# Optimization experiments

Measured on AMD Instinct MI355X. Metric: run time of the kernel, lower is better.

The kernel has to match this reference:

```python
import jax, jax.numpy as jnp
import numpy as np

C = 256
G = 32            # GroupNorm groups = min(32, C)
DQK = C // 8      # q/k channel dim
EPS = 1e-5


def setup_inputs() -> dict:
    key = jax.random.key(0)
    ks = jax.random.split(key, 10)
    B, H, W = 4, 64, 64
    s = 0.02
    return {
        "x": jax.random.normal(ks[0], (B, C, H, W), dtype=jnp.float32),
        "gamma": jnp.ones((C,), jnp.float32),
        "beta": jnp.zeros((C,), jnp.float32),
        "wq": jax.random.normal(ks[1], (DQK, C), jnp.float32) * s,
        "bq": jnp.zeros((DQK,), jnp.float32),
        "wk": jax.random.normal(ks[2], (DQK, C), jnp.float32) * s,
        "bk": jnp.zeros((DQK,), jnp.float32),
        "wv": jax.random.normal(ks[3], (C, C), jnp.float32) * s,
        "bv": jnp.zeros((C,), jnp.float32),
        "wp": jax.random.normal(ks[4], (C, C), jnp.float32) * s,
        "bp": jnpp if False else jnp.zeros((C,), jnp.float32),
    }


def reference(x, gamma, beta, wq, bq, wk, bk, wv, bv, wp, bp):
    B, Cc, H, W = x.shape
    N = H * W
    # GroupNorm(32, C), affine
    h = x.reshape(B, G, Cc // G, H, W)
    mu = h.mean(axis=(2, 3, 4), keepdims=True)
    var = h.var(axis=(2, 3, 4), keepdims=True)
    h = (h - mu) * jax.lax.rsqrt(var + EPS)
    h = h.reshape(B, Cc, N) * gamma[:, None] + beta[:, None]
    # 1x1 convs == per-token linear maps over channels
    q = jnp.einsum('dc,bcn->bnd', wq, h) + bq            # [B, N, DQK]
    k = jnp.einsum('dc,bcn->bdn', wk, h) + bk[:, None]   # [B, DQK, N]
    v = jnp.einsum('ec,bcn->ben', wv, h) + bv[:, None]   # [B, C, N]
    scale = DQK ** (-0.5)
    attn = jax.nn.softmax(jnp.einsum('bnd,bdm->bnm', q, k) * scale, axis=-1)
    out = jnp.einsum('bnm,bem->ben', attn, v)            # [B, C, N]
    proj = jnp.einsum('fe,ben->bfn', wp, out) + bp[:, None]
    return x + proj.reshape(B, Cc, H, W)
```

## Files before the change

### kernel.cpp

```cpp
#include <hip/hip_runtime.h>
#include <hip/hip_bf16.h>

#define NB 4
#define CD 256
#define NT 4096
#define DQ 32

typedef __attribute__((ext_vector_type(8))) __bf16 bf16x8;
typedef __attribute__((ext_vector_type(16))) float float16v;
typedef __attribute__((ext_vector_type(4))) unsigned int uint4v;
typedef __attribute__((ext_vector_type(2))) unsigned int uint2v;

#if __has_builtin(__builtin_amdgcn_exp2f)
#define EXP2(x) __builtin_amdgcn_exp2f(x)
#else
#define EXP2(x) exp2f(x)
#endif

__device__ inline unsigned short f2bf(float f) {
  unsigned u = __float_as_uint(f);
  u += 0x7fffu + ((u >> 16) & 1u);
  return (unsigned short)(u >> 16);
}

#define BARRIER() asm volatile("s_waitcnt lgkmcnt(0)\n\ts_barrier" ::: "memory")

__global__ __launch_bounds__(1024) void stats_pack(
    const float* __restrict__ x, const float* __restrict__ gamma,
    const float* __restrict__ beta, const float* __restrict__ wq,
    const float* __restrict__ wk, const float* __restrict__ wv,
    const float* __restrict__ wp, const float* __restrict__ bq,
    const float* __restrict__ bk, const float* __restrict__ bv,
    float* __restrict__ sc, float* __restrict__ sh,
    unsigned short* __restrict__ wqkv, unsigned short* __restrict__ wpb,
    float* __restrict__ bias) {
  int bx = blockIdx.x;
  int tid = threadIdx.x;
  if (bx < 128) {
    int b = bx >> 5, g = bx & 31;
    const float4* xp = (const float4*)(x + (size_t)bx * 32768);
    float s = 0.f, ss = 0.f;
#pragma unroll
    for (int i = 0; i < 8; i++) {
      float4 t4 = xp[i * 1024 + tid];
      s += t4.x + t4.y + t4.z + t4.w;
      ss += t4.x * t4.x + t4.y * t4.y + t4.z * t4.z + t4.w * t4.w;
    }
#pragma unroll
    for (int off = 32; off >= 1; off >>= 1) {
      s += __shfl_xor(s, off);
      ss += __shfl_xor(ss, off);
    }
    __shared__ float red[32];
    int wid = tid >> 6;
    if ((tid & 63) == 0) {
      red[wid] = s;
      red[16 + wid] = ss;
    }
    __syncthreads();
    if (tid < 8) {
      float S = 0.f, SS = 0.f;
#pragma unroll
      for (int i = 0; i < 16; i++) {
        S += red[i];
        SS += red[16 + i];
      }
      float mu = S * (1.f / 32768.f);
      float rstd = rsqrtf(SS * (1.f / 32768.f) - mu * mu + 1e-5f);
      int c = g * 8 + tid;
      float gm = gamma[c];
      sc[b * CD + c] = gm * rstd;
      sh[b * CD + c] = beta[c] - mu * gm * rstd;
    }
  } else {
    const float scale2 = 0.2550348909867343f;
    int i = (bx - 128) * 1024 + tid;
    if (i < 320 * 256) {
      int j = i >> 8, c = i & 255;
      float v;
      if (j < 32) v = wq[j * 256 + c] * scale2;
      else if (j < 64) v = wk[(j - 32) * 256 + c];
      else v = wv[(j - 64) * 256 + c];
      wqkv[i] = f2bf(v);
    } else if (i < 320 * 256 + 256 * 256) {
      int k = i - 320 * 256;
      wpb[k] = f2bf(wp[k]);
    } else if (i < 320 * 256 + 256 * 256 + 320) {
      int j = i - (320 * 256 + 256 * 256);
      float v;
      if (j < 32) v = bq[j] * scale2;
      else if (j < 64) v = bk[j - 32];
      else v = bv[j - 64];
      bias[j] = v;
    }
  }
}

__global__ __launch_bounds__(512) void qkv_norm(
    const float* __restrict__ x, const float* __restrict__ sc,
    const float* __restrict__ sh, const unsigned short* __restrict__ A,
    const float* __restrict__ bias, unsigned short* __restrict__ qk,
    unsigned short* __restrict__ v) {
  int nt = blockIdx.x, b = blockIdx.y;
  int tid = threadIdx.x, lane = tid & 63, w = tid >> 6;
  int l31 = lane & 31, hh = lane >> 5;
  int n0 = nt * 32;

  __shared__ unsigned short Hs[32 * 262];
  const float* xb = x + (size_t)b * CD * NT + n0;
  const float* scb = sc + b * CD;
  const float* shb = sh + b * CD;
  {
    int n_l = tid & 31, cg = tid >> 5;
    int c0 = cg * 16;
    unsigned short hv[16];
#pragma unroll
    for (int j = 0; j < 16; j++) {
      float val = xb[(size_t)(c0 + j) * NT + n_l];
      hv[j] = f2bf(val * scb[c0 + j] + shb[c0 + j]);
    }
    *(uint4v*)&Hs[n_l * 262 + c0] = *(uint4v*)hv;
    *(uint4v*)&Hs[n_l * 262 + c0 + 8] = *(uint4v*)(hv + 8);
  }
  __syncthreads();

  int n = n0 + l31;
  int itg = n >> 6, sp = (n >> 4) & 3;
  int lsn = ((n >> 3) & 1) * 32;
  int el = n & 7;
  const unsigned short* Brow = &Hs[l31 * 262 + 8 * hh];
  for (int t = w; t < 10; t += 8) {
    int m_base = t * 32;
    const unsigned short* Arow = A + (size_t)(m_base + l31) * 256 + 8 * hh;
    float16v acc;
#pragma unroll
    for (int r = 0; r < 16; r++) acc[r] = 0.f;
#pragma unroll
    for (int s = 0; s < 16; s++) {
      bf16x8 af = *(const bf16x8*)(Arow + 16 * s);
      bf16x8 bf = *(const bf16x8*)(Brow + 16 * s);
      acc = __builtin_amdgcn_mfma_f32_32x32x16_bf16(af, bf, acc, 0, 0, 0);
    }
#pragma unroll
    for (int r = 0; r < 16; r++) {
      int j = m_base + (r & 3) + 8 * (r >> 2) + 4 * hh;
      float val = acc[r] + bias[j];
      if (j < 64) {
        qk[((size_t)b * NT + n) * 64 + j] = f2bf(val);
      } else {
        int e = j - 64;
        int et = e >> 5;
        v[((((size_t)b * 64 + itg) * 8 + et) * 4 + sp) * 512 +
          (lsn + (e & 31)) * 8 + el] = f2bf(val);
      }
    }
  }
}

#define K_STAGE2(TNEXT, KSW)                                                  \
  if (tid >= 256) {                                                           \
    *(uint4v*)&Ks[(KSW) * 2304 + skr * 36 + skc] = kregA;                     \
    *(uint4v*)&Ks[((KSW) + 1) * 2304 + skr * 36 + skc] = kregB;               \
    int ta_ = (TNEXT) > 31 ? 31 : (TNEXT);                                    \
    int tb_ = (TNEXT) + 1 > 31 ? 31 : (TNEXT) + 1;                            \
    kregA =                                                                   \
        *(const uint4v*)&qkb[(size_t)(mbase + ta_ * 64 + skr) * 64 + 32 + skc]; \
    kregB =                                                                   \
        *(const uint4v*)&qkb[(size_t)(mbase + tb_ * 64 + skr) * 64 + 32 + skc]; \
  }

#define QK_ONE(KSB, PBB)                                                      \
  if (w < 4) {                                                                \
    float16v st;                                                              \
    _Pragma("unroll") for (int r = 0; r < 16; r++) st[r] = 0.f;               \
    __builtin_amdgcn_s_setprio(1);                                            \
    _Pragma("unroll") for (int s = 0; s < 2; s++) {                           \
      bf16x8 af = *(const bf16x8*)&Ks[(KSB) * 2304 + (32 * ks2 + l31) * 36 +  \
                                      16 * s + 8 * hh];                       \
      st = __builtin_amdgcn_mfma_f32_32x32x16_bf16(af, qfr[s], st, 0, 0, 0);  \
    }                                                                         \
    __builtin_amdgcn_s_setprio(0);                                            \
    _Pragma("unroll") for (int rq = 0; rq < 4; rq++) {                        \
      float e0 = EXP2(st[4 * rq + 0]);                                        \
      float e1 = EXP2(st[4 * rq + 1]);                                        \
      float e2 = EXP2(st[4 * rq + 2]);                                        \
      float e3 = EXP2(st[4 * rq + 3]);                                        \
      lsum += (e0 + e1) + (e2 + e3);                                          \
      uint2v pw;                                                              \
      pw[0] = __builtin_amdgcn_perm(__float_as_uint(e1), __float_as_uint(e0), \
                                    0x07060302u);                             \
      pw[1] = __builtin_amdgcn_perm(__float_as_uint(e3), __float_as_uint(e2), \
                                    0x07060302u);                             \
      *(uint2v*)&Pbuf[(PBB) * 4352 + (qs * 32 + l31) * 68 + 8 * rq + 4 * hh + \
                      32 * ks2] = pw;                                         \
    }                                                                         \
  }

#define PV_ONE(PBB, VS)                                                       \
  {                                                                           \
    __builtin_amdgcn_s_setprio(1);                                            \
    _Pragma("unroll") for (int sp = 0; sp < 4; sp++) {                        \
      bf16x8 a0 =                                                             \
          *(const bf16x8*)&Pbuf[(PBB) * 4352 + l31 * 68 + 16 * sp + 8 * hh];  \
      bf16x8 a1 = *(const bf16x8*)&Pbuf[(PBB) * 4352 + (32 + l31) * 68 +      \
                                        16 * sp + 8 * hh];                    \
      acc[0] =                                                                \
          __builtin_amdgcn_mfma_f32_32x32x16_bf16(a0, VS[sp], acc[0], 0, 0, 0); \
      acc[1] =                                                                \
          __builtin_amdgcn_mfma_f32_32x32x16_bf16(a1, VS[sp], acc[1], 0, 0, 0); \
    }                                                                         \
    __builtin_amdgcn_s_setprio(0);                                            \
  }

#define V_LOAD2(T)                                                            \
  {                                                                           \
    const unsigned short* vp0_ = vbase + (size_t)(T)*16384;                   \
    const unsigned short* vp1_ = vbase + (size_t)((T) + 1) * 16384;           \
    _Pragma("unroll") for (int u = 0; u < 4; u++) {                           \
      vS0[u] = *(const bf16x8*)(vp0_ + u * 512);                              \
      vS1[u] = *(const bf16x8*)(vp1_ + u * 512);                              \
    }                                                                         \
  }

__global__ __launch_bounds__(512, 4) void attn_fused(
    const unsigned short* __restrict__ qk, const unsigned short* __restrict__ Vp,
    unsigned short* __restrict__ Pa, unsigned short* __restrict__ Pb,
    float* __restrict__ lp4) {
  int L = blockIdx.x;
  int xv = L & 7;
  int b = xv >> 1;
  int kh = xv & 1;
  int n0 = (L >> 3) * 64;
  int tid = threadIdx.x, lane = tid & 63, w = tid >> 6;
  int l31 = lane & 31, hh = lane >> 5;
  int qs = w & 1, ks2 = (w >> 1) & 1;

  __shared__ unsigned short Ks[4 * 2304];
  __shared__ unsigned short Pbuf[4 * 4352];

  const unsigned short* qkb = qk + (size_t)b * NT * 64;
  const unsigned short* vit = Vp + ((size_t)b * 64 + kh * 32) * 16384;
  const unsigned short* vbase = vit + (size_t)w * 4 * 512 + lane * 8;

  bf16x8 qfr[2];
  if (w < 4) {
    int n_g = n0 + 32 * qs + l31;
    qfr[0] = *(const bf16x8*)&qkb[(size_t)n_g * 64 + 8 * hh];
    qfr[1] = *(const bf16x8*)&qkb[(size_t)n_g * 64 + 8 * hh + 16];
  }

  int tK = tid - 256;
  int skr = tK >> 2, skc = (tK & 3) * 8;
  int mbase = kh * 2048;
  uint4v kregA, kregB;

  float16v acc[2];
#pragma unroll
  for (int q2 = 0; q2 < 2; q2++)
#pragma unroll
    for (int r = 0; r < 16; r++) acc[q2][r] = 0.f;
  float lsum = 0.f;

  bf16x8 vS0[4], vS1[4];
  if (tid >= 256) {
    kregA = *(const uint4v*)&qkb[(size_t)(mbase + skr) * 64 + 32 + skc];
    kregB = *(const uint4v*)&qkb[(size_t)(mbase + 64 + skr) * 64 + 32 + skc];
    *(uint4v*)&Ks[skr * 36 + skc] = kregA;
    *(uint4v*)&Ks[2304 + skr * 36 + skc] = kregB;
    kregA = *(const uint4v*)&qkb[(size_t)(mbase + 128 + skr) * 64 + 32 + skc];
    kregB = *(const uint4v*)&qkb[(size_t)(mbase + 192 + skr) * 64 + 32 + skc];
  }
  BARRIER();

  K_STAGE2(4, 2);
  QK_ONE(0, 0);
  QK_ONE(1, 1);
  V_LOAD2(0);
  BARRIER();

  for (int p = 1; p < 15; p += 2) {
    K_STAGE2(2 * p + 4, 0);
    QK_ONE(2, 2);
    QK_ONE(3, 3);
    PV_ONE(0, vS0);
    PV_ONE(1, vS1);
    V_LOAD2(2 * p);
    BARRIER();
    K_STAGE2(2 * p + 6, 2);
    QK_ONE(0, 0);
    QK_ONE(1, 1);
    PV_ONE(2, vS0);
    PV_ONE(3, vS1);
    V_LOAD2(2 * p + 2);
    BARRIER();
  }
  K_STAGE2(34, 0);
  QK_ONE(2, 2);
  QK_ONE(3, 3);
  PV_ONE(0, vS0);
  PV_ONE(1, vS1);
  V_LOAD2(30);
  BARRIER();
  PV_ONE(2, vS0);
  PV_ONE(3, vS1);

  if (w < 4) {
    lsum += __shfl_xor(lsum, 32);
    if (hh == 0) {
      lp4[(size_t)((kh * 2 + ks2) * NB + b) * NT + n0 + 32 * qs + l31] = lsum;
    }
  }

  unsigned short* Pout = (kh ? Pb : Pa) + (size_t)b * NT * CD;
#pragma unroll
  for (int r = 0; r < 16; r++) {
    int nl = (r & 3) + 8 * (r >> 2) + 4 * hh;
    Pout[(size_t)(n0 + nl) * CD + 32 * w + l31] = f2bf(acc[0][r]);
    Pout[(size_t)(n0 + 32 + nl) * CD + 32 * w + l31] = f2bf(acc[1][r]);
  }
}

__global__ __launch_bounds__(256) void proj_gemm(
    const unsigned short* __restrict__ Wp, const unsigned short* __restrict__ Pa,
    const unsigned short* __restrict__ Pb, const float* __restrict__ lp4,
    const float* __restrict__ bp, const float* __restrict__ x,
    float* __restrict__ out) {
  int nt = blockIdx.x, mh = blockIdx.y, b = blockIdx.z;
  int tid = threadIdx.x, lane = tid & 63;
  int w = tid >> 6;
  int l31 = lane & 31, hh = lane >> 5;
  int n0 = nt * 32;

  __shared__ unsigned short Bs[32 * 262];
  {
    int row = tid >> 3, c8 = (tid & 7) * 8;
    float lA = 0.f;
#pragma unroll
    for (int s4 = 0; s4 < 4; s4++)
      lA += lp4[(size_t)(s4 * NB + b) * NT + n0 + row];
    float inv = 1.f / lA;
#pragma unroll
    for (int u = 0; u < 4; u++) {
      int col = c8 + u * 64;
      size_t goff = ((size_t)b * NT + n0 + row) * CD + col;
      uint4v ua = *(const uint4v*)(Pa + goff);
      uint4v ub = *(const uint4v*)(Pb + goff);
      uint4v rr;
#pragma unroll
      for (int j = 0; j < 4; j++) {
        float lo = __uint_as_float(ua[j] << 16) + __uint_as_float(ub[j] << 16);
        float hi = __uint_as_float(ua[j] & 0xffff0000u) +
                   __uint_as_float(ub[j] & 0xffff0000u);
        lo *= inv;
        hi *= inv;
        rr[j] = __builtin_amdgcn_perm(__float_as_uint(hi), __float_as_uint(lo),
                                      0x07060302u);
      }
      *(uint4v*)&Bs[row * 262 + col] = rr;
    }
  }
  __syncthreads();

  int m_base = mh * 128 + w * 32;
  const unsigned short* Arow = Wp + (size_t)(m_base + l31) * 256 + 8 * hh;
  const unsigned short* b0p = &Bs[l31 * 262 + 8 * hh];
  float16v acc;
#pragma unroll
  for (int r = 0; r < 16; r++) acc[r] = 0.f;
#pragma unroll
  for (int s = 0; s < 16; s++) {
    bf16x8 af = *(const bf16x8*)(Arow + 16 * s);
    bf16x8 bf0 = *(const bf16x8*)(b0p + 16 * s);
    acc = __builtin_amdgcn_mfma_f32_32x32x16_bf16(af, bf0, acc, 0, 0, 0);
  }
  int n = n0 + l31;
#pragma unroll
  for (int r = 0; r < 16; r++) {
    int f = m_base + (r & 3) + 8 * (r >> 2) + 4 * hh;
    size_t idx = ((size_t)b * CD + f) * NT + n;
    out[idx] = x[idx] + acc[r] + bp[f];
  }
}

extern "C" void kernel_launch(void* const* d_in, const int* in_sizes, int n_in,
                              void* d_out, int out_size, void* d_ws,
                              size_t ws_size, hipStream_t stream) {
  (void)in_sizes; (void)n_in; (void)out_size; (void)ws_size;
  const float* x = (const float*)d_in[0];
  const float* gamma = (const float*)d_in[1];
  const float* beta = (const float*)d_in[2];
  const float* wq = (const float*)d_in[3];
  const float* bq = (const float*)d_in[4];
  const float* wk = (const float*)d_in[5];
  const float* bk = (const float*)d_in[6];
  const float* wv = (const float*)d_in[7];
  const float* bv = (const float*)d_in[8];
  const float* wp = (const float*)d_in[9];
  const float* bp = (const float*)d_in[10];
  float* out = (float*)d_out;

  char* ws = (char*)d_ws;
  unsigned short* pa_ws = (unsigned short*)ws;
  unsigned short* qk_ws = (unsigned short*)(ws + 8388608);
  unsigned short* v_ws = (unsigned short*)(ws + 10485760);
  unsigned short* o_ws = (unsigned short*)(ws + 18874368);
  unsigned short* wqkv_b = (unsigned short*)(ws + 27262976);
  unsigned short* wp_b = (unsigned short*)(ws + 27426816);
  float* bias_q = (float*)(ws + 27557888);
  float* lp4 = (float*)(ws + 27563264);
  float* sc_ws = (float*)(ws + 27825408);
  float* sh_ws = (float*)(ws + 27829504);

  stats_pack<<<273, 1024, 0, stream>>>(x, gamma, beta, wq, wk, wv, wp, bq, bk,
                                       bv, sc_ws, sh_ws, wqkv_b, wp_b, bias_q);
  dim3 gq(128, NB);
  qkv_norm<<<gq, 512, 0, stream>>>(x, sc_ws, sh_ws, wqkv_b, bias_q, qk_ws,
                                   v_ws);
  attn_fused<<<512, 512, 0, stream>>>(qk_ws, v_ws, pa_ws, o_ws, lp4);
  dim3 gp(128, 2, NB);
  proj_gemm<<<gp, 256, 0, stream>>>(wp_b, pa_ws, o_ws, lp4, bp, x, out);
}
```

Before: 169.5 us.

## Double attention block to 1024 threads, splitting PV accumulation across query halves

The fused attention kernel now launches 1024 threads per block instead of 512. Each wave handles one 32-row query half of the PV product (a single accumulator instead of two). K staging is spread across 512 threads, one register each, instead of 256 threads holding two. The aim is more waves in flight for latency hiding and lower per-thread register pressure. In exchange, every V fragment is loaded twice (once per query half), and the launch bounds of (1024, 8) may not be satisfiable, which could force register spills.

```diff
diff --git a/kernel.cpp b/kernel.cpp
--- a/kernel.cpp
+++ b/kernel.cpp
@@ -158,15 +158,12 @@
 }
 
 #define K_STAGE2(TNEXT, KSW)                                                  \
-  if (tid >= 256) {                                                           \
-    *(uint4v*)&Ks[(KSW) * 2304 + skr * 36 + skc] = kregA;                     \
-    *(uint4v*)&Ks[((KSW) + 1) * 2304 + skr * 36 + skc] = kregB;               \
-    int ta_ = (TNEXT) > 31 ? 31 : (TNEXT);                                    \
-    int tb_ = (TNEXT) + 1 > 31 ? 31 : (TNEXT) + 1;                            \
-    kregA =                                                                   \
-        *(const uint4v*)&qkb[(size_t)(mbase + ta_ * 64 + skr) * 64 + 32 + skc]; \
-    kregB =                                                                   \
-        *(const uint4v*)&qkb[(size_t)(mbase + tb_ * 64 + skr) * 64 + 32 + skc]; \
+  if (tid >= 512) {                                                           \
+    *(uint4v*)&Ks[((KSW) + ksel) * 2304 + skr * 36 + skc] = kreg;             \
+    int ta_ = (TNEXT) + ksel;                                                 \
+    if (ta_ > 31) ta_ = 31;                                                   \
+    kreg = *(const uint4v*)&qkb[(size_t)(mbase + ta_ * 64 + skr) * 64 + 32 +  \
+                                skc];                                         \
   }
 
 #define QK_ONE(KSB, PBB)                                                      \
@@ -200,14 +197,10 @@
   {                                                                           \
     __builtin_amdgcn_s_setprio(1);                                            \
     _Pragma("unroll") for (int sp = 0; sp < 4; sp++) {                        \
-      bf16x8 a0 =                                                             \
-          *(const bf16x8*)&Pbuf[(PBB) * 4352 + l31 * 68 + 16 * sp + 8 * hh];  \
-      bf16x8 a1 = *(const bf16x8*)&Pbuf[(PBB) * 4352 + (32 + l31) * 68 +      \
+      bf16x8 a0 = *(const bf16x8*)&Pbuf[(PBB) * 4352 + (qh * 32 + l31) * 68 + \
                                         16 * sp + 8 * hh];                    \
-      acc[0] =                                                                \
-          __builtin_amdgcn_mfma_f32_32x32x16_bf16(a0, VS[sp], acc[0], 0, 0, 0); \
-      acc[1] =                                                                \
-          __builtin_amdgcn_mfma_f32_32x32x16_bf16(a1, VS[sp], acc[1], 0, 0, 0); \
+      acc =                                                                   \
+          __builtin_amdgcn_mfma_f32_32x32x16_bf16(a0, VS[sp], acc, 0, 0, 0);  \
     }                                                                         \
     __builtin_amdgcn_s_setprio(0);                                            \
   }
@@ -222,7 +215,7 @@
     }                                                                         \
   }
 
-__global__ __launch_bounds__(512, 4) void attn_fused(
+__global__ __launch_bounds__(1024, 8) void attn_fused(
     const unsigned short* __restrict__ qk, const unsigned short* __restrict__ Vp,
     unsigned short* __restrict__ Pa, unsigned short* __restrict__ Pb,
     float* __restrict__ lp4) {
@@ -234,13 +227,14 @@
   int tid = threadIdx.x, lane = tid & 63, w = tid >> 6;
   int l31 = lane & 31, hh = lane >> 5;
   int qs = w & 1, ks2 = (w >> 1) & 1;
+  int qh = w >> 3, we = w & 7;
 
   __shared__ unsigned short Ks[4 * 2304];
   __shared__ unsigned short Pbuf[4 * 4352];
 
   const unsigned short* qkb = qk + (size_t)b * NT * 64;
   const unsigned short* vit = Vp + ((size_t)b * 64 + kh * 32) * 16384;
-  const unsigned short* vbase = vit + (size_t)w * 4 * 512 + lane * 8;
+  const unsigned short* vbase = vit + (size_t)we * 4 * 512 + lane * 8;
 
   bf16x8 qfr[2];
   if (w < 4) {
@@ -249,26 +243,24 @@
     qfr[1] = *(const bf16x8*)&qkb[(size_t)n_g * 64 + 8 * hh + 16];
   }
 
-  int tK = tid - 256;
-  int skr = tK >> 2, skc = (tK & 3) * 8;
+  int tK = tid - 512;
+  int ksel = tK >> 8;
+  int skr = (tK & 255) >> 2, skc = (tK & 3) * 8;
   int mbase = kh * 2048;
-  uint4v kregA, kregB;
-
-  float16v acc[2];
-#pragma unroll
-  for (int q2 = 0; q2 < 2; q2++)
-#pragma unroll
-    for (int r = 0; r < 16; r++) acc[q2][r] = 0.f;
+  uint4v kreg;
+
+  float16v acc;
+#pragma unroll
+  for (int r = 0; r < 16; r++) acc[r] = 0.f;
   float lsum = 0.f;
 
   bf16x8 vS0[4], vS1[4];
-  if (tid >= 256) {
-    kregA = *(const uint4v*)&qkb[(size_t)(mbase + skr) * 64 + 32 + skc];
-    kregB = *(const uint4v*)&qkb[(size_t)(mbase + 64 + skr) * 64 + 32 + skc];
-    *(uint4v*)&Ks[skr * 36 + skc] = kregA;
-    *(uint4v*)&Ks[2304 + skr * 36 + skc] = kregB;
-    kregA = *(const uint4v*)&qkb[(size_t)(mbase + 128 + skr) * 64 + 32 + skc];
-    kregB = *(const uint4v*)&qkb[(size_t)(mbase + 192 + skr) * 64 + 32 + skc];
+  if (tid >= 512) {
+    kreg = *(const uint4v*)&qkb[(size_t)(mbase + ksel * 64 + skr) * 64 + 32 +
+                                skc];
+    *(uint4v*)&Ks[ksel * 2304 + skr * 36 + skc] = kreg;
+    kreg = *(const uint4v*)&qkb[(size_t)(mbase + (2 + ksel) * 64 + skr) * 64 +
+                                32 + skc];
   }
   BARRIER();
 
@@ -315,8 +307,7 @@
 #pragma unroll
   for (int r = 0; r < 16; r++) {
     int nl = (r & 3) + 8 * (r >> 2) + 4 * hh;
-    Pout[(size_t)(n0 + nl) * CD + 32 * w + l31] = f2bf(acc[0][r]);
-    Pout[(size_t)(n0 + 32 + nl) * CD + 32 * w + l31] = f2bf(acc[1][r]);
+    Pout[(size_t)(n0 + qh * 32 + nl) * CD + 32 * we + l31] = f2bf(acc[r]);
   }
 }
 
@@ -416,7 +407,7 @@
   dim3 gq(128, NB);
   qkv_norm<<<gq, 512, 0, stream>>>(x, sc_ws, sh_ws, wqkv_b, bias_q, qk_ws,
                                    v_ws);
-  attn_fused<<<512, 512, 0, stream>>>(qk_ws, v_ws, pa_ws, o_ws, lp4);
+  attn_fused<<<512, 1024, 0, stream>>>(qk_ws, v_ws, pa_ws, o_ws, lp4);
   dim3 gp(128, 2, NB);
   proj_gemm<<<gp, 256, 0, stream>>>(wp_b, pa_ws, o_ws, lp4, bp, x, out);
 }
```

Result: slower. 405.1 us (+138.9%).

## Halve attention query tile to 32 rows and double grid for occupancy

Applied to the files above, without the earlier changes.

The fused attention kernel now handles 32 query rows per block instead of 64 and launches 1024 blocks. The four QK waves are remapped so each computes one of two key tiles times one key-half, and the partial row sums grow from 4 to 8 slots, which proj_gemm now adds up. This halves the accumulator registers and the P buffer in shared memory, so more blocks can be resident (launch bounds raised to 8) and the GPU gets more parallelism. The cost is that every K and V tile is loaded twice as often from global memory or L2, with less reuse per load.

```diff
diff --git a/kernel.cpp b/kernel.cpp
--- a/kernel.cpp
+++ b/kernel.cpp
@@ -169,13 +169,14 @@
         *(const uint4v*)&qkb[(size_t)(mbase + tb_ * 64 + skr) * 64 + 32 + skc]; \
   }
 
-#define QK_ONE(KSB, PBB)                                                      \
+#define QK_PAIR(BASE)                                                         \
   if (w < 4) {                                                                \
+    int qb_ = (BASE) + tp;                                                    \
     float16v st;                                                              \
     _Pragma("unroll") for (int r = 0; r < 16; r++) st[r] = 0.f;               \
     __builtin_amdgcn_s_setprio(1);                                            \
     _Pragma("unroll") for (int s = 0; s < 2; s++) {                           \
-      bf16x8 af = *(const bf16x8*)&Ks[(KSB) * 2304 + (32 * ks2 + l31) * 36 +  \
+      bf16x8 af = *(const bf16x8*)&Ks[qb_ * 2304 + (32 * ks2 + l31) * 36 +    \
                                       16 * s + 8 * hh];                       \
       st = __builtin_amdgcn_mfma_f32_32x32x16_bf16(af, qfr[s], st, 0, 0, 0);  \
     }                                                                         \
@@ -191,8 +192,8 @@
                                     0x07060302u);                             \
       pw[1] = __builtin_amdgcn_perm(__float_as_uint(e3), __float_as_uint(e2), \
                                     0x07060302u);                             \
-      *(uint2v*)&Pbuf[(PBB) * 4352 + (qs * 32 + l31) * 68 + 8 * rq + 4 * hh + \
-                      32 * ks2] = pw;                                         \
+      *(uint2v*)&Pbuf[qb_ * 2176 + l31 * 68 + 8 * rq + 4 * hh + 32 * ks2] =   \
+          pw;                                                                 \
     }                                                                         \
   }
 
@@ -200,14 +201,10 @@
   {                                                                           \
     __builtin_amdgcn_s_setprio(1);                                            \
     _Pragma("unroll") for (int sp = 0; sp < 4; sp++) {                        \
-      bf16x8 a0 =                                                             \
-          *(const bf16x8*)&Pbuf[(PBB) * 4352 + l31 * 68 + 16 * sp + 8 * hh];  \
-      bf16x8 a1 = *(const bf16x8*)&Pbuf[(PBB) * 4352 + (32 + l31) * 68 +      \
-                                        16 * sp + 8 * hh];                    \
-      acc[0] =                                                                \
-          __builtin_amdgcn_mfma_f32_32x32x16_bf16(a0, VS[sp], acc[0], 0, 0, 0); \
-      acc[1] =                                                                \
-          __builtin_amdgcn_mfma_f32_32x32x16_bf16(a1, VS[sp], acc[1], 0, 0, 0); \
+      bf16x8 a0 = *(const bf16x8*)&Pbuf[(PBB) * 2176 + l31 * 68 + 16 * sp +   \
+                                        8 * hh];                              \
+      acc =                                                                   \
+          __builtin_amdgcn_mfma_f32_32x32x16_bf16(a0, VS[sp], acc, 0, 0, 0);  \
     }                                                                         \
     __builtin_amdgcn_s_setprio(0);                                            \
   }
@@ -222,21 +219,21 @@
     }                                                                         \
   }
 
-__global__ __launch_bounds__(512, 4) void attn_fused(
+__global__ __launch_bounds__(512, 8) void attn_fused(
     const unsigned short* __restrict__ qk, const unsigned short* __restrict__ Vp,
     unsigned short* __restrict__ Pa, unsigned short* __restrict__ Pb,
-    float* __restrict__ lp4) {
+    float* __restrict__ lp8) {
   int L = blockIdx.x;
   int xv = L & 7;
   int b = xv >> 1;
   int kh = xv & 1;
-  int n0 = (L >> 3) * 64;
+  int n0 = (L >> 3) * 32;
   int tid = threadIdx.x, lane = tid & 63, w = tid >> 6;
   int l31 = lane & 31, hh = lane >> 5;
-  int qs = w & 1, ks2 = (w >> 1) & 1;
+  int tp = (w >> 1) & 1, ks2 = w & 1;
 
   __shared__ unsigned short Ks[4 * 2304];
-  __shared__ unsigned short Pbuf[4 * 4352];
+  __shared__ unsigned short Pbuf[4 * 2176];
 
   const unsigned short* qkb = qk + (size_t)b * NT * 64;
   const unsigned short* vit = Vp + ((size_t)b * 64 + kh * 32) * 16384;
@@ -244,7 +241,7 @@
 
   bf16x8 qfr[2];
   if (w < 4) {
-    int n_g = n0 + 32 * qs + l31;
+    int n_g = n0 + l31;
     qfr[0] = *(const bf16x8*)&qkb[(size_t)n_g * 64 + 8 * hh];
     qfr[1] = *(const bf16x8*)&qkb[(size_t)n_g * 64 + 8 * hh + 16];
   }
@@ -254,11 +251,9 @@
   int mbase = kh * 2048;
   uint4v kregA, kregB;
 
-  float16v acc[2];
-#pragma unroll
-  for (int q2 = 0; q2 < 2; q2++)
-#pragma unroll
-    for (int r = 0; r < 16; r++) acc[q2][r] = 0.f;
+  float16v acc;
+#pragma unroll
+  for (int r = 0; r < 16; r++) acc[r] = 0.f;
   float lsum = 0.f;
 
   bf16x8 vS0[4], vS1[4];
@@ -273,30 +268,26 @@
   BARRIER();
 
   K_STAGE2(4, 2);
-  QK_ONE(0, 0);
-  QK_ONE(1, 1);
+  QK_PAIR(0);
   V_LOAD2(0);
   BARRIER();
 
   for (int p = 1; p < 15; p += 2) {
     K_STAGE2(2 * p + 4, 0);
-    QK_ONE(2, 2);
-    QK_ONE(3, 3);
+    QK_PAIR(2);
     PV_ONE(0, vS0);
     PV_ONE(1, vS1);
     V_LOAD2(2 * p);
     BARRIER();
     K_STAGE2(2 * p + 6, 2);
-    QK_ONE(0, 0);
-    QK_ONE(1, 1);
+    QK_PAIR(0);
     PV_ONE(2, vS0);
     PV_ONE(3, vS1);
     V_LOAD2(2 * p + 2);
     BARRIER();
   }
   K_STAGE2(34, 0);
-  QK_ONE(2, 2);
-  QK_ONE(3, 3);
+  QK_PAIR(2);
   PV_ONE(0, vS0);
   PV_ONE(1, vS1);
   V_LOAD2(30);
@@ -307,7 +298,7 @@
   if (w < 4) {
     lsum += __shfl_xor(lsum, 32);
     if (hh == 0) {
-      lp4[(size_t)((kh * 2 + ks2) * NB + b) * NT + n0 + 32 * qs + l31] = lsum;
+      lp8[(size_t)((kh * 4 + w) * NB + b) * NT + n0 + l31] = lsum;
     }
   }
 
@@ -315,14 +306,13 @@
 #pragma unroll
   for (int r = 0; r < 16; r++) {
     int nl = (r & 3) + 8 * (r >> 2) + 4 * hh;
-    Pout[(size_t)(n0 + nl) * CD + 32 * w + l31] = f2bf(acc[0][r]);
-    Pout[(size_t)(n0 + 32 + nl) * CD + 32 * w + l31] = f2bf(acc[1][r]);
+    Pout[(size_t)(n0 + nl) * CD + 32 * w + l31] = f2bf(acc[r]);
   }
 }
 
 __global__ __launch_bounds__(256) void proj_gemm(
     const unsigned short* __restrict__ Wp, const unsigned short* __restrict__ Pa,
-    const unsigned short* __restrict__ Pb, const float* __restrict__ lp4,
+    const unsigned short* __restrict__ Pb, const float* __restrict__ lp8,
     const float* __restrict__ bp, const float* __restrict__ x,
     float* __restrict__ out) {
   int nt = blockIdx.x, mh = blockIdx.y, b = blockIdx.z;
@@ -336,8 +326,8 @@
     int row = tid >> 3, c8 = (tid & 7) * 8;
     float lA = 0.f;
 #pragma unroll
-    for (int s4 = 0; s4 < 4; s4++)
-      lA += lp4[(size_t)(s4 * NB + b) * NT + n0 + row];
+    for (int s4 = 0; s4 < 8; s4++)
+      lA += lp8[(size_t)(s4 * NB + b) * NT + n0 + row];
     float inv = 1.f / lA;
 #pragma unroll
     for (int u = 0; u < 4; u++) {
@@ -407,16 +397,16 @@
   unsigned short* wqkv_b = (unsigned short*)(ws + 27262976);
   unsigned short* wp_b = (unsigned short*)(ws + 27426816);
   float* bias_q = (float*)(ws + 27557888);
-  float* lp4 = (float*)(ws + 27563264);
-  float* sc_ws = (float*)(ws + 27825408);
-  float* sh_ws = (float*)(ws + 27829504);
+  float* lp8 = (float*)(ws + 27563264);
+  float* sc_ws = (float*)(ws + 28087552);
+  float* sh_ws = (float*)(ws + 28091648);
 
   stats_pack<<<273, 1024, 0, stream>>>(x, gamma, beta, wq, wk, wv, wp, bq, bk,
                                        bv, sc_ws, sh_ws, wqkv_b, wp_b, bias_q);
   dim3 gq(128, NB);
   qkv_norm<<<gq, 512, 0, stream>>>(x, sc_ws, sh_ws, wqkv_b, bias_q, qk_ws,
                                    v_ws);
-  attn_fused<<<512, 512, 0, stream>>>(qk_ws, v_ws, pa_ws, o_ws, lp4);
+  attn_fused<<<1024, 512, 0, stream>>>(qk_ws, v_ws, pa_ws, o_ws, lp8);
   dim3 gp(128, 2, NB);
-  proj_gemm<<<gp, 256, 0, stream>>>(wp_b, pa_ws, o_ws, lp4, bp, x, out);
-}
+  proj_gemm<<<gp, 256, 0, stream>>>(wp_b, pa_ws, o_ws, lp8, bp, x, out);
+}
```

Result: slower. 392.8 us (+131.7%).
